# Optimization experiments

Measured on AMD Instinct MI355X. Metric: run time of the kernel, lower is better.

The kernel has to match this reference:

```python
import jax, jax.numpy as jnp
import numpy as np

B, ORDER, N, D, H = 16, 2, 512, 128, 8
DH = D // H
NEG_SLOPE = 0.2


def setup_inputs() -> dict:
    key = jax.random.key(0)
    ks = jax.random.split(key, 8)
    stdv = 1.0 / np.sqrt(DH)

    def u(k, shape):
        return jax.random.uniform(k, shape, jnp.float32, -stdv, stdv)

    x = jax.random.normal(ks[0], (B, ORDER, N, D), jnp.float32)
    A = jax.random.randint(ks[1], (B, ORDER, N, N), 0, 5, jnp.int32)
    # Stacked params for the 2*order GAT modules: axis0 = order, axis1 = (conv1, conv2)
    W = u(ks[2], (ORDER, 2, D, D))            # project.weight
    pb = jnp.zeros((ORDER, 2, D), jnp.float32)  # project.bias (init 0)
    att_src = u(ks[3], (ORDER, 2, H, DH))
    att_dst = u(ks[4], (ORDER, 2, H, DH))
    bias = jnp.zeros((ORDER, 2, D), jnp.float32)  # GAT output bias (init 0)
    return {"x": x, "A": A, "W": W, "pb": pb,
            "att_src": att_src, "att_dst": att_dst, "bias": bias}


def _gat(x, Af, W, pb, a_src, a_dst, b):
    # x: [B,N,D]; Af: [B,N,N] float in {0,1}
    xp = x @ W.T + pb                                  # project
    xh = xp.reshape(B, N, H, DH)                       # [B,N,H,DH]
    s_src = jnp.einsum('bnhd,hd->bnh', xh, a_src)      # [B,N,H]
    s_dst = jnp.einsum('bnhd,hd->bnh', xh, a_dst)
    alpha = s_src[:, :, None, :] + s_dst[:, None, :, :]  # [B,src,dst,H]
    alpha = jnp.where((Af != 1.0)[..., None], 0.0, alpha)
    alpha = jnp.where(alpha >= 0, alpha, NEG_SLOPE * alpha)  # leaky relu
    alpha = jax.nn.softmax(alpha, axis=1)              # softmax over src dim
    out = jnp.einsum('bsdh,bshf->bdhf', alpha, xh).reshape(B, N, D)
    out = out + xp                                     # add_self_loops
    return out + b


def reference(x, A, W, pb, att_src, att_dst, bias):
    A1 = ((A == 2) | (A == 4)).astype(x.dtype)  # [B,ORDER,N,N]
    A2 = ((A == 3) | (A == 4)).astype(x.dtype)
    hs = []
    for i in range(ORDER):
        h1 = _gat(x[:, i], A1[:, i], W[i, 0], pb[i, 0], att_src[i, 0], att_dst[i, 0], bias[i, 0])
        h2 = _gat(x[:, i], A2[:, i], W[i, 1], pb[i, 1], att_src[i, 1], att_dst[i, 1], bias[i, 1])
        hs.append(h1 + h2)
    h = jnp.stack(hs, axis=1)                          # [B,ORDER,N,D]
    out = h + h.mean(axis=1, keepdims=True)
    return out
```

## Files before the change

kernel.cpp:

```cpp
#include <hip/hip_runtime.h>

#define N_ 512
#define D_ 128
#define LOG2E 1.44269504088896f


typedef __attribute__((ext_vector_type(8))) short short8;
typedef __attribute__((ext_vector_type(4))) float floatx4;
typedef __attribute__((ext_vector_type(4))) unsigned int uintx4;
typedef __attribute__((ext_vector_type(2))) _Float16 half2v;
typedef __attribute__((ext_vector_type(8))) _Float16 half8;

#if defined(__has_builtin)
#if __has_builtin(__builtin_amdgcn_exp2f)
#define EXP2F(x) __builtin_amdgcn_exp2f(x)
#else
#define EXP2F(x) exp2f(x)
#endif
#else
#define EXP2F(x) exp2f(x)
#endif

__device__ __forceinline__ unsigned int pkh(float a, float b) {
    auto h = __builtin_amdgcn_cvt_pkrtz(a, b);
    return __builtin_bit_cast(unsigned int, h);
}

__global__ __launch_bounds__(256) void prep_kernel(
    const float* __restrict__ x, const float* __restrict__ W,
    const float* __restrict__ pb, const float* __restrict__ att_src,
    const float* __restrict__ att_dst, const int* __restrict__ A,
    unsigned short* __restrict__ xpt, unsigned int* __restrict__ sgEs,
    unsigned int* __restrict__ sgFs, float2* __restrict__ sgD,
    unsigned int* __restrict__ mgT)
{
    __shared__ _Float16 va_l[8][136];
    __shared__ float c0_l[8];

    const int bid0 = blockIdx.x;
    const int t = threadIdx.x;

    if (bid0 >= 1024) {
        const int bid = bid0 - 1024;
        const int bi = bid >> 4;
        const int rem = bid & 15;
        const int dg = rem >> 2;
        const int jw = rem & 3;
        const int dp = t & 63, q = t >> 6;
        const int dstb = dg * 128 + dp * 2;
        const int sbase = jw * 128 + q * 8;
        const int* Ab = A + (size_t)bi * N_ * N_ + dstb;
        unsigned int a00 = 0, a01 = 0, a10 = 0, a11 = 0;
#pragma unroll
        for (int cp = 0; cp < 4; ++cp) {
#pragma unroll
            for (int i = 0; i < 8; ++i) {
                const int s = sbase + cp * 32 + i;
                const int2 v = *(const int2*)(Ab + (size_t)s * N_);
                const int bitp = cp * 8 + i;
                a00 |= ((0x14u >> v.x) & 1u) << bitp;
                a10 |= ((0x18u >> v.x) & 1u) << bitp;
                a01 |= ((0x14u >> v.y) & 1u) << bitp;
                a11 |= ((0x18u >> v.y) & 1u) << bitp;
            }
        }
        const int i0 = bi * 2;
        mgT[(((size_t)i0 * 4 + q) * 512 + dstb + 0) * 4 + jw] = a00;
        mgT[(((size_t)i0 * 4 + q) * 512 + dstb + 1) * 4 + jw] = a01;
        mgT[(((size_t)(i0 + 1) * 4 + q) * 512 + dstb + 0) * 4 + jw] = a10;
        mgT[(((size_t)(i0 + 1) * 4 + q) * 512 + dstb + 1) * 4 + jw] = a11;
        return;
    }

    const int unit = bid0 >> 1;
    const int half = bid0 & 1;
    const int ntile = unit & 7;
    const int inst  = unit >> 3;
    const int j = inst & 1;
    const int bi = inst >> 1;
    const int ij = (bi & 1) * 2 + j;
    const int wave = t >> 6, L = t & 63, n = L & 15, q = L >> 4;
    const float* wb = W + (size_t)ij * D_ * D_;

    {
        const int c = t >> 5;
        const int k0 = (t & 31) * 4;
        const int hn = half * 4 + (c & 3);
        const float* av = ((c < 4) ? att_src : att_dst) + ij * D_ + hn * 16;
        const float* Wh = wb + (size_t)(hn * 16) * D_ + k0;
        float a0 = 0.f, a1 = 0.f, a2 = 0.f, a3 = 0.f;
#pragma unroll
        for (int dd = 0; dd < 16; ++dd) {
            const float a = av[dd];
            const float4 wv = *(const float4*)(Wh + (size_t)dd * D_);
            a0 += wv.x * a; a1 += wv.y * a; a2 += wv.z * a; a3 += wv.w * a;
        }
        va_l[c][k0 + 0] = (_Float16)(a0 * LOG2E);
        va_l[c][k0 + 1] = (_Float16)(a1 * LOG2E);
        va_l[c][k0 + 2] = (_Float16)(a2 * LOG2E);
        va_l[c][k0 + 3] = (_Float16)(a3 * LOG2E);
        if (t < 8) {
            const int hn2 = half * 4 + (t & 3);
            const float* av2 = ((t < 4) ? att_src : att_dst) + ij * D_ + hn2 * 16;
            const float* pbp = pb + ij * D_ + hn2 * 16;
            float s = 0.f;
#pragma unroll
            for (int dd = 0; dd < 16; ++dd) s += pbp[dd] * av2[dd];
            c0_l[t] = s * LOG2E;
        }
    }

    const int n0w = ntile * 64 + wave * 16;
    const float* xrow = x + ((size_t)bi * N_ + n0w + n) * D_ + q * 8;
    half8 Af[4];
#pragma unroll
    for (int kc = 0; kc < 4; ++kc) {
        const float4 a0 = *(const float4*)(xrow + kc * 32);
        const float4 a1 = *(const float4*)(xrow + kc * 32 + 4);
        uintx4 au;
        au.x = pkh(a0.x, a0.y);
        au.y = pkh(a0.z, a0.w);
        au.z = pkh(a1.x, a1.y);
        au.w = pkh(a1.z, a1.w);
        Af[kc] = __builtin_bit_cast(half8, au);
    }

    __syncthreads();

    floatx4 S = (floatx4){0.f, 0.f, 0.f, 0.f};
    {
        const _Float16* var = &va_l[n & 7][q * 8];
#pragma unroll
        for (int kc = 0; kc < 4; ++kc) {
            const half8 Bs = *(const half8*)(var + kc * 32);
            S = __builtin_amdgcn_mfma_f32_16x16x32_f16(Af[kc], Bs, S, 0, 0, 0);
        }
    }

#pragma unroll
    for (int ft = 0; ft < 4; ++ft) {
        const int head = half * 4 + ft;
        const int fg = head * 16 + n;
        const float* wrow = wb + (size_t)fg * D_ + q * 8;
        floatx4 C = (floatx4){0.f, 0.f, 0.f, 0.f};
#pragma unroll
        for (int kc = 0; kc < 4; ++kc) {
            const float4 b0 = *(const float4*)(wrow + kc * 32);
            const float4 b1 = *(const float4*)(wrow + kc * 32 + 4);
            uintx4 bu;
            bu.x = pkh(b0.x, b0.y);
            bu.y = pkh(b0.z, b0.w);
            bu.z = pkh(b1.x, b1.y);
            bu.w = pkh(b1.z, b1.w);
            C = __builtin_amdgcn_mfma_f32_16x16x32_f16(
                Af[kc], __builtin_bit_cast(half8, bu), C, 0, 0, 0);
        }
        const float pbv = pb[ij * D_ + fg];
        uint2 pk;
        pk.x = pkh(C[0] + pbv, C[1] + pbv);
        pk.y = pkh(C[2] + pbv, C[3] + pbv);
        *(uint2*)&xpt[((size_t)inst * D_ + fg) * N_ + n0w + q * 4] = pk;
    }

    if (n < 8) {
        const float cc = c0_l[n];
        const float v0 = S[0] + cc, v1 = S[1] + cc;
        const float v2 = S[2] + cc, v3 = S[3] + cc;
        if (n < 4) {
            const int head = half * 4 + n;
            const size_t base = ((size_t)inst * 8 + head) * 256 + (n0w >> 1) + q * 2;
            sgEs[base + 0] = pkh(EXP2F(v0), EXP2F(v1));
            sgEs[base + 1] = pkh(EXP2F(v2), EXP2F(v3));
            sgFs[base + 0] = pkh(EXP2F(0.2f * v0), EXP2F(0.2f * v1));
            sgFs[base + 1] = pkh(EXP2F(0.2f * v2), EXP2F(0.2f * v3));
        } else {
            const int head = half * 4 + (n - 4);
            const size_t base = ((size_t)inst * 8 + head) * N_ + n0w + q * 4;
            float2 e0; e0.x = EXP2F(v0); e0.y = EXP2F(0.2f * v0); sgD[base + 0] = e0;
            float2 e1; e1.x = EXP2F(v1); e1.y = EXP2F(0.2f * v1); sgD[base + 1] = e1;
            float2 e2; e2.x = EXP2F(v2); e2.y = EXP2F(0.2f * v2); sgD[base + 2] = e2;
            float2 e3; e3.x = EXP2F(v3); e3.y = EXP2F(0.2f * v3); sgD[base + 3] = e3;
        }
    }
}

__global__ __launch_bounds__(1024, 4) void attn_kernel(
    const unsigned short* __restrict__ xpt,
    const unsigned int* __restrict__ sgEs,
    const unsigned int* __restrict__ sgFs,
    const float2* __restrict__ sgD,
    const unsigned int* __restrict__ mgT,
    const float* __restrict__ bias,
    float* __restrict__ hout)
{
    __shared__ unsigned int smem[16384];

    const int bid = blockIdx.x;
    const int xcd = bid & 7;
    const int idx = bid >> 3;
    const int b   = xcd * 2 + (idx >> 4);
    const int tp  = idx & 15;
    const int d0a = tp * 32;
    const int b4  = b * 4;
    const int t = threadIdx.x;
    const int wave = t >> 6, L = t & 63, n = L & 15, q = L >> 4;
    const int io = wave >> 3;
    const int cv = (wave >> 2) & 1;
    const int h0 = (wave & 3) * 2;
    const int il = io * 2 + cv;
    const int inst = b4 + il;
    const int ij = il;

    const int ph = tp & 3;
    const int Pb = ph * 128;

    {
        const uint4* sE = (const uint4*)(sgEs + (size_t)b4 * 2048);
        const uint4* sF = (const uint4*)(sgFs + (size_t)b4 * 2048);
        uint4* dE = (uint4*)smem;
        uint4* dF = (uint4*)(smem + 8192);
        dE[t] = sE[t]; dE[1024 + t] = sE[1024 + t];
        dF[t] = sF[t]; dF[1024 + t] = sF[1024 + t];
    }

    unsigned int mwr[2][4];
    unsigned int iEd2[2][2], rd2[2][2];
#pragma unroll
    for (int tt = 0; tt < 2; ++tt) {
        const int d0 = d0a + tt * 16;
        const uint4 mreg =
            *(const uint4*)(mgT + (((size_t)inst * 4 + q) * 512 + d0 + n) * 4);
        const unsigned int mwt[4] = { mreg.x, mreg.y, mreg.z, mreg.w };
#pragma unroll
        for (int w = 0; w < 4; ++w) {
            const int src = (w + ph) & 3;
            unsigned int v = mwt[0];
            v = (src == 1) ? mwt[1] : v;
            v = (src == 2) ? mwt[2] : v;
            v = (src == 3) ? mwt[3] : v;
            mwr[tt][w] = v;
        }
#pragma unroll
        for (int hh = 0; hh < 2; ++hh) {
            const float2 ed = sgD[((size_t)inst * 8 + h0 + hh) * N_ + d0 + n];
            const float iEd = 1.0f / ed.x;
            const float rdv = ed.y * iEd;
            iEd2[tt][hh] = pkh(iEd, iEd);
            rd2[tt][hh] = pkh(rdv, rdv);
        }
    }

    __syncthreads();

    const unsigned short* xpi = xpt + (size_t)inst * D_ * N_;
    const unsigned short* bpq0 = xpi + (size_t)(h0 * 16 + n) * N_ + q * 8;
    const unsigned short* bpq1 = xpi + (size_t)((h0 + 1) * 16 + n) * N_ + q * 8;
    const unsigned int* esw = smem + il * 2048;
    const unsigned int* fsw = smem + 8192 + il * 2048;
    const unsigned int* e0p = esw + h0 * 256 + q * 4;
    const unsigned int* e1p = esw + (h0 + 1) * 256 + q * 4;
    const unsigned int* f0p = fsw + h0 * 256 + q * 4;
    const unsigned int* f1p = fsw + (h0 + 1) * 256 + q * 4;

    const uintx4 ou = { 0x3C003C00u, 0x3C003C00u, 0x3C003C00u, 0x3C003C00u };
    const half8 onesB = __builtin_bit_cast(half8, ou);

    floatx4 Cacc[2][2] = { { (floatx4){0.f,0.f,0.f,0.f}, (floatx4){0.f,0.f,0.f,0.f} },
                           { (floatx4){0.f,0.f,0.f,0.f}, (floatx4){0.f,0.f,0.f,0.f} } };
    floatx4 Cz[2][2]   = { { (floatx4){0.f,0.f,0.f,0.f}, (floatx4){0.f,0.f,0.f,0.f} },
                           { (floatx4){0.f,0.f,0.f,0.f}, (floatx4){0.f,0.f,0.f,0.f} } };

    uintx4 Bb0[4], Bb1[4];
#pragma unroll
    for (int c = 0; c < 4; ++c) {
        const int off = (c * 32 + Pb) & 511;
        Bb0[c] = *(const uintx4*)(bpq0 + off);
        Bb1[c] = *(const uintx4*)(bpq1 + off);
    }
#pragma unroll
    for (int c = 0; c < 16; ++c) {
        const int offe = (c * 16 + (Pb >> 1)) & 255;
#pragma unroll
        for (int hh = 0; hh < 2; ++hh) {
            const uint4 Ep = *(const uint4*)((hh ? e1p : e0p) + offe);
            const uint4 Fp = *(const uint4*)((hh ? f1p : f0p) + offe);
            const unsigned int eu[4] = { Ep.x, Ep.y, Ep.z, Ep.w };
            const unsigned int fu[4] = { Fp.x, Fp.y, Fp.z, Fp.w };
            const half8 Bc = __builtin_bit_cast(half8, hh ? Bb1[c & 3] : Bb0[c & 3]);
#pragma unroll
            for (int tt = 0; tt < 2; ++tt) {
                const half2v rdh = __builtin_bit_cast(half2v, rd2[tt][hh]);
                const unsigned int word = mwr[tt][c >> 2];
                uintx4 au;
                unsigned int wts[4];
#pragma unroll
                for (int p = 0; p < 4; ++p) {
                    const int sh = (c & 3) * 8 + 2 * p;
                    const unsigned int wb2 = word >> sh;
                    const unsigned int sel =
                        ((wb2 & 1u) ? 0x0000FFFFu : 0u) |
                        ((wb2 & 2u) ? 0xFFFF0000u : 0u);
                    const half2v e = __builtin_bit_cast(half2v, eu[p]);
                    const half2v f = __builtin_bit_cast(half2v, fu[p]);
                    const half2v pr = f * rdh;
                    const half2v wv = __builtin_elementwise_max(pr, e);
                    const unsigned int wvu = __builtin_bit_cast(unsigned int, wv);
                    wts[p] = (sel & wvu) | (~sel & iEd2[tt][hh]);
                }
                au.x = wts[0]; au.y = wts[1]; au.z = wts[2]; au.w = wts[3];
                const half8 As = __builtin_bit_cast(half8, au);
                Cacc[tt][hh] = __builtin_amdgcn_mfma_f32_16x16x32_f16(
                    As, Bc, Cacc[tt][hh], 0, 0, 0);
                Cz[tt][hh] = __builtin_amdgcn_mfma_f32_16x16x32_f16(
                    As, onesB, Cz[tt][hh], 0, 0, 0);
            }
        }
        if (c < 12) {
            const int off = ((c + 4) * 32 + Pb) & 511;
            Bb0[c & 3] = *(const uintx4*)(bpq0 + off);
            Bb1[c & 3] = *(const uintx4*)(bpq1 + off);
        }
    }

    float vals[2][2][4];
#pragma unroll
    for (int tt = 0; tt < 2; ++tt) {
        const int d0 = d0a + tt * 16;
#pragma unroll
        for (int hh = 0; hh < 2; ++hh) {
            const int h = h0 + hh;
            const float bv = bias[ij * D_ + h * 16 + n];
            const uint2 sv =
                *(const uint2*)(xpi + (size_t)(h * 16 + n) * N_ + d0 + q * 4);
            const half2v s0 = __builtin_bit_cast(half2v, sv.x);
            const half2v s1 = __builtin_bit_cast(half2v, sv.y);
            const float selfv[4] = { (float)s0[0], (float)s0[1],
                                     (float)s1[0], (float)s1[1] };
#pragma unroll
            for (int reg = 0; reg < 4; ++reg) {
                const float Zi = 1.0f / Cz[tt][hh][reg];
                vals[tt][hh][reg] = Cacc[tt][hh][reg] * Zi + selfv[reg] + bv;
            }
        }
    }

    __syncthreads();
    float* smf = (float*)smem;
    if (cv == 1) {
#pragma unroll
        for (int tt = 0; tt < 2; ++tt) {
            float* out_l = smf + (tt * 2 + io) * 2112;
#pragma unroll
            for (int hh = 0; hh < 2; ++hh)
#pragma unroll
                for (int reg = 0; reg < 4; ++reg)
                    out_l[(q * 4 + reg) * 132 + (h0 + hh) * 16 + n] =
                        vals[tt][hh][reg];
        }
    }
    __syncthreads();
    if (cv == 0) {
#pragma unroll
        for (int tt = 0; tt < 2; ++tt) {
            float* out_l = smf + (tt * 2 + io) * 2112;
#pragma unroll
            for (int hh = 0; hh < 2; ++hh)
#pragma unroll
                for (int reg = 0; reg < 4; ++reg) {
                    vals[tt][hh][reg] +=
                        out_l[(q * 4 + reg) * 132 + (h0 + hh) * 16 + n];
                    out_l[(q * 4 + reg) * 132 + (h0 + hh) * 16 + n] =
                        vals[tt][hh][reg];
                }
        }
    }
    __syncthreads();
    if (cv == 0) {
#pragma unroll
        for (int tt = 0; tt < 2; ++tt) {
            const int d0 = d0a + tt * 16;
            const float* oth = smf + (tt * 2 + (1 - io)) * 2112;
#pragma unroll
            for (int hh = 0; hh < 2; ++hh)
#pragma unroll
                for (int reg = 0; reg < 4; ++reg) {
                    const float other =
                        oth[(q * 4 + reg) * 132 + (h0 + hh) * 16 + n];
                    hout[((size_t)(b * 2 + io) * N_ + d0 + q * 4 + reg) * D_ +
                         (h0 + hh) * 16 + n] =
                        1.5f * vals[tt][hh][reg] + 0.5f * other;
                }
        }
    }
}

extern "C" void kernel_launch(void* const* d_in, const int* in_sizes, int n_in,
                              void* d_out, int out_size, void* d_ws, size_t ws_size,
                              hipStream_t stream)
{
    const float* x   = (const float*)d_in[0];
    const int*   A   = (const int*)d_in[1];
    const float* W   = (const float*)d_in[2];
    const float* pb  = (const float*)d_in[3];
    const float* as_ = (const float*)d_in[4];
    const float* ad_ = (const float*)d_in[5];
    const float* bs  = (const float*)d_in[6];

    unsigned short* xpt = (unsigned short*)d_ws;
    unsigned int* sgEs = (unsigned int*)((char*)d_ws + (8u << 20));
    unsigned int* sgFs = (unsigned int*)((char*)d_ws + (8u << 20) + (512u << 10));
    float2* sgD = (float2*)((char*)d_ws + (9u << 20));
    unsigned int* mgT = (unsigned int*)((char*)d_ws + (11u << 20));
    float* h = (float*)d_out;

    prep_kernel<<<1536, 256, 0, stream>>>(x, W, pb, as_, ad_, A, xpt, sgEs, sgFs, sgD, mgT);
    attn_kernel<<<256, 1024, 0, stream>>>(xpt, sgEs, sgFs, sgD, mgT, bs, h);
}
```

Before: 132.1 us.

## Fuse prep and attention kernels into one cooperative launch with grid sync

Merges the projection/score/mask-packing prep kernel and the attention kernel into a single cooperative kernel of 256 blocks of 1024 threads. The prep work is redistributed across the larger blocks, and the attention phase presumably runs after a grid-wide sync. Mask loads now use nontemporal 64-bit loads. This removes one kernel launch and the gap between kernels. In exchange it adds a grid barrier, and the prep phase now runs at the lower parallelism of the attention launch shape.

```diff
diff --git a/kernel.cpp b/kernel.cpp
--- a/kernel.cpp
+++ b/kernel.cpp
@@ -1,8 +1,11 @@
 #include <hip/hip_runtime.h>
+#include <hip/hip_cooperative_groups.h>
 
 #define N_ 512
 #define D_ 128
 #define LOG2E 1.44269504088896f
+
+namespace cg = cooperative_groups;
 
 
 typedef __attribute__((ext_vector_type(8))) short short8;
@@ -26,370 +29,376 @@
     return __builtin_bit_cast(unsigned int, h);
 }
 
-__global__ __launch_bounds__(256) void prep_kernel(
+__global__ __launch_bounds__(1024, 4) void fused_kernel(
     const float* __restrict__ x, const float* __restrict__ W,
     const float* __restrict__ pb, const float* __restrict__ att_src,
     const float* __restrict__ att_dst, const int* __restrict__ A,
+    const float* __restrict__ bias,
     unsigned short* __restrict__ xpt, unsigned int* __restrict__ sgEs,
     unsigned int* __restrict__ sgFs, float2* __restrict__ sgD,
-    unsigned int* __restrict__ mgT)
-{
-    __shared__ _Float16 va_l[8][136];
-    __shared__ float c0_l[8];
-
-    const int bid0 = blockIdx.x;
-    const int t = threadIdx.x;
-
-    if (bid0 >= 1024) {
-        const int bid = bid0 - 1024;
-        const int bi = bid >> 4;
-        const int rem = bid & 15;
-        const int dg = rem >> 2;
-        const int jw = rem & 3;
-        const int dp = t & 63, q = t >> 6;
-        const int dstb = dg * 128 + dp * 2;
-        const int sbase = jw * 128 + q * 8;
-        const int* Ab = A + (size_t)bi * N_ * N_ + dstb;
-        unsigned int a00 = 0, a01 = 0, a10 = 0, a11 = 0;
-#pragma unroll
-        for (int cp = 0; cp < 4; ++cp) {
-#pragma unroll
-            for (int i = 0; i < 8; ++i) {
-                const int s = sbase + cp * 32 + i;
-                const int2 v = *(const int2*)(Ab + (size_t)s * N_);
-                const int bitp = cp * 8 + i;
-                a00 |= ((0x14u >> v.x) & 1u) << bitp;
-                a10 |= ((0x18u >> v.x) & 1u) << bitp;
-                a01 |= ((0x14u >> v.y) & 1u) << bitp;
-                a11 |= ((0x18u >> v.y) & 1u) << bitp;
-            }
-        }
-        const int i0 = bi * 2;
-        mgT[(((size_t)i0 * 4 + q) * 512 + dstb + 0) * 4 + jw] = a00;
-        mgT[(((size_t)i0 * 4 + q) * 512 + dstb + 1) * 4 + jw] = a01;
-        mgT[(((size_t)(i0 + 1) * 4 + q) * 512 + dstb + 0) * 4 + jw] = a10;
-        mgT[(((size_t)(i0 + 1) * 4 + q) * 512 + dstb + 1) * 4 + jw] = a11;
-        return;
-    }
-
-    const int unit = bid0 >> 1;
-    const int half = bid0 & 1;
-    const int ntile = unit & 7;
-    const int inst  = unit >> 3;
-    const int j = inst & 1;
-    const int bi = inst >> 1;
-    const int ij = (bi & 1) * 2 + j;
-    const int wave = t >> 6, L = t & 63, n = L & 15, q = L >> 4;
-    const float* wb = W + (size_t)ij * D_ * D_;
-
-    {
-        const int c = t >> 5;
-        const int k0 = (t & 31) * 4;
-        const int hn = half * 4 + (c & 3);
-        const float* av = ((c < 4) ? att_src : att_dst) + ij * D_ + hn * 16;
-        const float* Wh = wb + (size_t)(hn * 16) * D_ + k0;
-        float a0 = 0.f, a1 = 0.f, a2 = 0.f, a3 = 0.f;
-#pragma unroll
-        for (int dd = 0; dd < 16; ++dd) {
-            const float a = av[dd];
-            const float4 wv = *(const float4*)(Wh + (size_t)dd * D_);
-            a0 += wv.x * a; a1 += wv.y * a; a2 += wv.z * a; a3 += wv.w * a;
-        }
-        va_l[c][k0 + 0] = (_Float16)(a0 * LOG2E);
-        va_l[c][k0 + 1] = (_Float16)(a1 * LOG2E);
-        va_l[c][k0 + 2] = (_Float16)(a2 * LOG2E);
-        va_l[c][k0 + 3] = (_Float16)(a3 * LOG2E);
-        if (t < 8) {
-            const int hn2 = half * 4 + (t & 3);
-            const float* av2 = ((t < 4) ? att_src : att_dst) + ij * D_ + hn2 * 16;
-            const float* pbp = pb + ij * D_ + hn2 * 16;
-            float s = 0.f;
-#pragma unroll
-            for (int dd = 0; dd < 16; ++dd) s += pbp[dd] * av2[dd];
-            c0_l[t] = s * LOG2E;
-        }
-    }
-
-    const int n0w = ntile * 64 + wave * 16;
-    const float* xrow = x + ((size_t)bi * N_ + n0w + n) * D_ + q * 8;
-    half8 Af[4];
-#pragma unroll
-    for (int kc = 0; kc < 4; ++kc) {
-        const float4 a0 = *(const float4*)(xrow + kc * 32);
-        const float4 a1 = *(const float4*)(xrow + kc * 32 + 4);
-        uintx4 au;
-        au.x = pkh(a0.x, a0.y);
-        au.y = pkh(a0.z, a0.w);
-        au.z = pkh(a1.x, a1.y);
-        au.w = pkh(a1.z, a1.w);
-        Af[kc] = __builtin_bit_cast(half8, au);
-    }
-
-    __syncthreads();
-
-    floatx4 S = (floatx4){0.f, 0.f, 0.f, 0.f};
-    {
-        const _Float16* var = &va_l[n & 7][q * 8];
-#pragma unroll
-        for (int kc = 0; kc < 4; ++kc) {
-            const half8 Bs = *(const half8*)(var + kc * 32);
-            S = __builtin_amdgcn_mfma_f32_16x16x32_f16(Af[kc], Bs, S, 0, 0, 0);
-        }
-    }
-
-#pragma unroll
-    for (int ft = 0; ft < 4; ++ft) {
-        const int head = half * 4 + ft;
-        const int fg = head * 16 + n;
-        const float* wrow = wb + (size_t)fg * D_ + q * 8;
-        floatx4 C = (floatx4){0.f, 0.f, 0.f, 0.f};
-#pragma unroll
-        for (int kc = 0; kc < 4; ++kc) {
-            const float4 b0 = *(const float4*)(wrow + kc * 32);
-            const float4 b1 = *(const float4*)(wrow + kc * 32 + 4);
-            uintx4 bu;
-            bu.x = pkh(b0.x, b0.y);
-            bu.y = pkh(b0.z, b0.w);
-            bu.z = pkh(b1.x, b1.y);
-            bu.w = pkh(b1.z, b1.w);
-            C = __builtin_amdgcn_mfma_f32_16x16x32_f16(
-                Af[kc], __builtin_bit_cast(half8, bu), C, 0, 0, 0);
-        }
-        const float pbv = pb[ij * D_ + fg];
-        uint2 pk;
-        pk.x = pkh(C[0] + pbv, C[1] + pbv);
-        pk.y = pkh(C[2] + pbv, C[3] + pbv);
-        *(uint2*)&xpt[((size_t)inst * D_ + fg) * N_ + n0w + q * 4] = pk;
-    }
-
-    if (n < 8) {
-        const float cc = c0_l[n];
-        const float v0 = S[0] + cc, v1 = S[1] + cc;
-        const float v2 = S[2] + cc, v3 = S[3] + cc;
-        if (n < 4) {
-            const int head = half * 4 + n;
-            const size_t base = ((size_t)inst * 8 + head) * 256 + (n0w >> 1) + q * 2;
-            sgEs[base + 0] = pkh(EXP2F(v0), EXP2F(v1));
-            sgEs[base + 1] = pkh(EXP2F(v2), EXP2F(v3));
-            sgFs[base + 0] = pkh(EXP2F(0.2f * v0), EXP2F(0.2f * v1));
-            sgFs[base + 1] = pkh(EXP2F(0.2f * v2), EXP2F(0.2f * v3));
-        } else {
-            const int head = half * 4 + (n - 4);
-            const size_t base = ((size_t)inst * 8 + head) * N_ + n0w + q * 4;
-            float2 e0; e0.x = EXP2F(v0); e0.y = EXP2F(0.2f * v0); sgD[base + 0] = e0;
-            float2 e1; e1.x = EXP2F(v1); e1.y = EXP2F(0.2f * v1); sgD[base + 1] = e1;
-            float2 e2; e2.x = EXP2F(v2); e2.y = EXP2F(0.2f * v2); sgD[base + 2] = e2;
-            float2 e3; e3.x = EXP2F(v3); e3.y = EXP2F(0.2f * v3); sgD[base + 3] = e3;
-        }
-    }
-}
-
-__global__ __launch_bounds__(1024, 4) void attn_kernel(
-    const unsigned short* __restrict__ xpt,
-    const unsigned int* __restrict__ sgEs,
-    const unsigned int* __restrict__ sgFs,
-    const float2* __restrict__ sgD,
-    const unsigned int* __restrict__ mgT,
-    const float* __restrict__ bias,
-    float* __restrict__ hout)
+    unsigned int* __restrict__ mgT, float* __restrict__ hout)
 {
     __shared__ unsigned int smem[16384];
 
     const int bid = blockIdx.x;
     const int xcd = bid & 7;
     const int idx = bid >> 3;
-    const int b   = xcd * 2 + (idx >> 4);
-    const int tp  = idx & 15;
-    const int d0a = tp * 32;
-    const int b4  = b * 4;
     const int t = threadIdx.x;
-    const int wave = t >> 6, L = t & 63, n = L & 15, q = L >> 4;
-    const int io = wave >> 3;
-    const int cv = (wave >> 2) & 1;
-    const int h0 = (wave & 3) * 2;
-    const int il = io * 2 + cv;
-    const int inst = b4 + il;
-    const int ij = il;
-
-    const int ph = tp & 3;
-    const int Pb = ph * 128;
 
     {
-        const uint4* sE = (const uint4*)(sgEs + (size_t)b4 * 2048);
-        const uint4* sF = (const uint4*)(sgFs + (size_t)b4 * 2048);
-        uint4* dE = (uint4*)smem;
-        uint4* dF = (uint4*)(smem + 8192);
-        dE[t] = sE[t]; dE[1024 + t] = sE[1024 + t];
-        dF[t] = sF[t]; dF[1024 + t] = sF[1024 + t];
+        const int inst = xcd * 8 + (idx >> 2);
+        const int quarter = idx & 3;
+        const int j = inst & 1;
+        const int bi = inst >> 1;
+        const int ij = (bi & 1) * 2 + j;
+        const float* wb = W + (size_t)ij * D_ * D_;
+
+        _Float16* va = (_Float16*)smem;
+        float* c0s = (float*)(smem + 1100);
+
+        if (t < 512) {
+            const int halfv = t >> 8;
+            const int c = (t >> 5) & 7;
+            const int k0 = (t & 31) * 4;
+            const int hn = halfv * 4 + (c & 3);
+            const float* av = ((c < 4) ? att_src : att_dst) + ij * D_ + hn * 16;
+            const float* Wh = wb + (size_t)(hn * 16) * D_ + k0;
+            float a0 = 0.f, a1 = 0.f, a2 = 0.f, a3 = 0.f;
+#pragma unroll
+            for (int dd = 0; dd < 16; ++dd) {
+                const float a = av[dd];
+                const float4 wv = *(const float4*)(Wh + (size_t)dd * D_);
+                a0 += wv.x * a; a1 += wv.y * a; a2 += wv.z * a; a3 += wv.w * a;
+            }
+            _Float16* vp = va + (halfv * 8 + c) * 136 + k0;
+            vp[0] = (_Float16)(a0 * LOG2E);
+            vp[1] = (_Float16)(a1 * LOG2E);
+            vp[2] = (_Float16)(a2 * LOG2E);
+            vp[3] = (_Float16)(a3 * LOG2E);
+        }
+        if (t < 16) {
+            const int halfv = t >> 3;
+            const int cc = t & 7;
+            const int hn2 = halfv * 4 + (cc & 3);
+            const float* av2 = ((cc < 4) ? att_src : att_dst) + ij * D_ + hn2 * 16;
+            const float* pbp = pb + ij * D_ + hn2 * 16;
+            float s = 0.f;
+#pragma unroll
+            for (int dd = 0; dd < 16; ++dd) s += pbp[dd] * av2[dd];
+            c0s[halfv * 8 + cc] = s * LOG2E;
+        }
+
+        const int sub = t >> 8;
+        const int ntile = quarter * 2 + (sub >> 1);
+        const int halfp = sub & 1;
+        const int wavep = (t >> 6) & 3;
+        const int L = t & 63, n = L & 15, q = L >> 4;
+        const int n0w = ntile * 64 + wavep * 16;
+
+        const float* xrow = x + ((size_t)bi * N_ + n0w + n) * D_ + q * 8;
+        half8 Af[4];
+#pragma unroll
+        for (int kc = 0; kc < 4; ++kc) {
+            const float4 a0 = *(const float4*)(xrow + kc * 32);
+            const float4 a1 = *(const float4*)(xrow + kc * 32 + 4);
+            uintx4 au;
+            au.x = pkh(a0.x, a0.y);
+            au.y = pkh(a0.z, a0.w);
+            au.z = pkh(a1.x, a1.y);
+            au.w = pkh(a1.z, a1.w);
+            Af[kc] = __builtin_bit_cast(half8, au);
+        }
+
+        __syncthreads();
+
+        floatx4 S = (floatx4){0.f, 0.f, 0.f, 0.f};
+        {
+            const _Float16* var = va + (halfp * 8 + (n & 7)) * 136 + q * 8;
+#pragma unroll
+            for (int kc = 0; kc < 4; ++kc) {
+                const half8 Bs = *(const half8*)(var + kc * 32);
+                S = __builtin_amdgcn_mfma_f32_16x16x32_f16(Af[kc], Bs, S, 0, 0, 0);
+            }
+        }
+
+#pragma unroll
+        for (int ft = 0; ft < 4; ++ft) {
+            const int head = halfp * 4 + ft;
+            const int fg = head * 16 + n;
+            const float* wrow = wb + (size_t)fg * D_ + q * 8;
+            floatx4 C = (floatx4){0.f, 0.f, 0.f, 0.f};
+#pragma unroll
+            for (int kc = 0; kc < 4; ++kc) {
+                const float4 b0 = *(const float4*)(wrow + kc * 32);
+                const float4 b1 = *(const float4*)(wrow + kc * 32 + 4);
+                uintx4 bu;
+                bu.x = pkh(b0.x, b0.y);
+                bu.y = pkh(b0.z, b0.w);
+                bu.z = pkh(b1.x, b1.y);
+                bu.w = pkh(b1.z, b1.w);
+                C = __builtin_amdgcn_mfma_f32_16x16x32_f16(
+                    Af[kc], __builtin_bit_cast(half8, bu), C, 0, 0, 0);
+            }
+            const float pbv = pb[ij * D_ + fg];
+            uint2 pk;
+            pk.x = pkh(C[0] + pbv, C[1] + pbv);
+            pk.y = pkh(C[2] + pbv, C[3] + pbv);
+            *(uint2*)&xpt[((size_t)inst * D_ + fg) * N_ + n0w + q * 4] = pk;
+        }
+
+        if (n < 8) {
+            const float cc2 = c0s[halfp * 8 + n];
+            const float v0 = S[0] + cc2, v1 = S[1] + cc2;
+            const float v2 = S[2] + cc2, v3 = S[3] + cc2;
+            if (n < 4) {
+                const int head = halfp * 4 + n;
+                const size_t base = ((size_t)inst * 8 + head) * 256 + (n0w >> 1) + q * 2;
+                sgEs[base + 0] = pkh(EXP2F(v0), EXP2F(v1));
+                sgEs[base + 1] = pkh(EXP2F(v2), EXP2F(v3));
+                sgFs[base + 0] = pkh(EXP2F(0.2f * v0), EXP2F(0.2f * v1));
+                sgFs[base + 1] = pkh(EXP2F(0.2f * v2), EXP2F(0.2f * v3));
+            } else {
+                const int head = halfp * 4 + (n - 4);
+                const size_t base = ((size_t)inst * 8 + head) * N_ + n0w + q * 4;
+                float2 e0; e0.x = EXP2F(v0); e0.y = EXP2F(0.2f * v0); sgD[base + 0] = e0;
+                float2 e1; e1.x = EXP2F(v1); e1.y = EXP2F(0.2f * v1); sgD[base + 1] = e1;
+                float2 e2; e2.x = EXP2F(v2); e2.y = EXP2F(0.2f * v2); sgD[base + 2] = e2;
+                float2 e3; e3.x = EXP2F(v3); e3.y = EXP2F(0.2f * v3); sgD[base + 3] = e3;
+            }
+        }
+
+        if (t < 512) {
+            const int sub2 = t >> 8;
+            const int u = idx * 2 + sub2;
+            const int bim = xcd * 4 + (u >> 4);
+            const int rem = u & 15;
+            const int dg = rem >> 2, jw = rem & 3;
+            const int tl = t & 255;
+            const int qm = tl >> 6, dp = tl & 63;
+            const int dstb = dg * 128 + dp * 2;
+            const int sbase = jw * 128 + qm * 8;
+            const long long* Ab =
+                (const long long*)(A + (size_t)bim * N_ * N_ + dstb);
+            unsigned int a00 = 0, a01 = 0, a10 = 0, a11 = 0;
+#pragma unroll
+            for (int cp = 0; cp < 4; ++cp) {
+#pragma unroll
+                for (int i = 0; i < 8; ++i) {
+                    const int s = sbase + cp * 32 + i;
+                    const long long vv =
+                        __builtin_nontemporal_load(Ab + (size_t)s * (N_ / 2));
+                    const unsigned int vx = (unsigned int)(vv & 0xffffffffll);
+                    const unsigned int vy = (unsigned int)(vv >> 32);
+                    const int bitp = cp * 8 + i;
+                    a00 |= ((0x14u >> vx) & 1u) << bitp;
+                    a10 |= ((0x18u >> vx) & 1u) << bitp;
+                    a01 |= ((0x14u >> vy) & 1u) << bitp;
+                    a11 |= ((0x18u >> vy) & 1u) << bitp;
+                }
+            }
+            const int i0 = bim * 2;
+            mgT[(((size_t)i0 * 4 + qm) * 512 + dstb + 0) * 4 + jw] = a00;
+            mgT[(((size_t)i0 * 4 + qm) * 512 + dstb + 1) * 4 + jw] = a01;
+            mgT[(((size_t)(i0 + 1) * 4 + qm) * 512 + dstb + 0) * 4 + jw] = a10;
+            mgT[(((size_t)(i0 + 1) * 4 + qm) * 512 + dstb + 1) * 4 + jw] = a11;
+        }
     }
 
-    unsigned int mwr[2][4];
-    unsigned int iEd2[2][2], rd2[2][2];
-#pragma unroll
-    for (int tt = 0; tt < 2; ++tt) {
-        const int d0 = d0a + tt * 16;
-        const uint4 mreg =
-            *(const uint4*)(mgT + (((size_t)inst * 4 + q) * 512 + d0 + n) * 4);
-        const unsigned int mwt[4] = { mreg.x, mreg.y, mreg.z, mreg.w };
-#pragma unroll
-        for (int w = 0; w < 4; ++w) {
-            const int src = (w + ph) & 3;
-            unsigned int v = mwt[0];
-            v = (src == 1) ? mwt[1] : v;
-            v = (src == 2) ? mwt[2] : v;
-            v = (src == 3) ? mwt[3] : v;
-            mwr[tt][w] = v;
-        }
-#pragma unroll
-        for (int hh = 0; hh < 2; ++hh) {
-            const float2 ed = sgD[((size_t)inst * 8 + h0 + hh) * N_ + d0 + n];
-            const float iEd = 1.0f / ed.x;
-            const float rdv = ed.y * iEd;
-            iEd2[tt][hh] = pkh(iEd, iEd);
-            rd2[tt][hh] = pkh(rdv, rdv);
-        }
-    }
-
-    __syncthreads();
-
-    const unsigned short* xpi = xpt + (size_t)inst * D_ * N_;
-    const unsigned short* bpq0 = xpi + (size_t)(h0 * 16 + n) * N_ + q * 8;
-    const unsigned short* bpq1 = xpi + (size_t)((h0 + 1) * 16 + n) * N_ + q * 8;
-    const unsigned int* esw = smem + il * 2048;
-    const unsigned int* fsw = smem + 8192 + il * 2048;
-    const unsigned int* e0p = esw + h0 * 256 + q * 4;
-    const unsigned int* e1p = esw + (h0 + 1) * 256 + q * 4;
-    const unsigned int* f0p = fsw + h0 * 256 + q * 4;
-    const unsigned int* f1p = fsw + (h0 + 1) * 256 + q * 4;
-
-    const uintx4 ou = { 0x3C003C00u, 0x3C003C00u, 0x3C003C00u, 0x3C003C00u };
-    const half8 onesB = __builtin_bit_cast(half8, ou);
-
-    floatx4 Cacc[2][2] = { { (floatx4){0.f,0.f,0.f,0.f}, (floatx4){0.f,0.f,0.f,0.f} },
-                           { (floatx4){0.f,0.f,0.f,0.f}, (floatx4){0.f,0.f,0.f,0.f} } };
-    floatx4 Cz[2][2]   = { { (floatx4){0.f,0.f,0.f,0.f}, (floatx4){0.f,0.f,0.f,0.f} },
-                           { (floatx4){0.f,0.f,0.f,0.f}, (floatx4){0.f,0.f,0.f,0.f} } };
-
-    uintx4 Bb0[4], Bb1[4];
-#pragma unroll
-    for (int c = 0; c < 4; ++c) {
-        const int off = (c * 32 + Pb) & 511;
-        Bb0[c] = *(const uintx4*)(bpq0 + off);
-        Bb1[c] = *(const uintx4*)(bpq1 + off);
-    }
-#pragma unroll
-    for (int c = 0; c < 16; ++c) {
-        const int offe = (c * 16 + (Pb >> 1)) & 255;
-#pragma unroll
-        for (int hh = 0; hh < 2; ++hh) {
-            const uint4 Ep = *(const uint4*)((hh ? e1p : e0p) + offe);
-            const uint4 Fp = *(const uint4*)((hh ? f1p : f0p) + offe);
-            const unsigned int eu[4] = { Ep.x, Ep.y, Ep.z, Ep.w };
-            const unsigned int fu[4] = { Fp.x, Fp.y, Fp.z, Fp.w };
-            const half8 Bc = __builtin_bit_cast(half8, hh ? Bb1[c & 3] : Bb0[c & 3]);
-#pragma unroll
-            for (int tt = 0; tt < 2; ++tt) {
-                const half2v rdh = __builtin_bit_cast(half2v, rd2[tt][hh]);
-                const unsigned int word = mwr[tt][c >> 2];
-                uintx4 au;
-                unsigned int wts[4];
-#pragma unroll
-                for (int p = 0; p < 4; ++p) {
-                    const int sh = (c & 3) * 8 + 2 * p;
-                    const unsigned int wb2 = word >> sh;
-                    const unsigned int sel =
-                        ((wb2 & 1u) ? 0x0000FFFFu : 0u) |
-                        ((wb2 & 2u) ? 0xFFFF0000u : 0u);
-                    const half2v e = __builtin_bit_cast(half2v, eu[p]);
-                    const half2v f = __builtin_bit_cast(half2v, fu[p]);
-                    const half2v pr = f * rdh;
-                    const half2v wv = __builtin_elementwise_max(pr, e);
-                    const unsigned int wvu = __builtin_bit_cast(unsigned int, wv);
-                    wts[p] = (sel & wvu) | (~sel & iEd2[tt][hh]);
-                }
-                au.x = wts[0]; au.y = wts[1]; au.z = wts[2]; au.w = wts[3];
-                const half8 As = __builtin_bit_cast(half8, au);
-                Cacc[tt][hh] = __builtin_amdgcn_mfma_f32_16x16x32_f16(
-                    As, Bc, Cacc[tt][hh], 0, 0, 0);
-                Cz[tt][hh] = __builtin_amdgcn_mfma_f32_16x16x32_f16(
-                    As, onesB, Cz[tt][hh], 0, 0, 0);
-            }
-        }
-        if (c < 12) {
-            const int off = ((c + 4) * 32 + Pb) & 511;
-            Bb0[c & 3] = *(const uintx4*)(bpq0 + off);
-            Bb1[c & 3] = *(const uintx4*)(bpq1 + off);
-        }
-    }
-
-    float vals[2][2][4];
-#pragma unroll
-    for (int tt = 0; tt < 2; ++tt) {
-        const int d0 = d0a + tt * 16;
-#pragma unroll
-        for (int hh = 0; hh < 2; ++hh) {
-            const int h = h0 + hh;
-            const float bv = bias[ij * D_ + h * 16 + n];
-            const uint2 sv =
-                *(const uint2*)(xpi + (size_t)(h * 16 + n) * N_ + d0 + q * 4);
-            const half2v s0 = __builtin_bit_cast(half2v, sv.x);
-            const half2v s1 = __builtin_bit_cast(half2v, sv.y);
-            const float selfv[4] = { (float)s0[0], (float)s0[1],
-                                     (float)s1[0], (float)s1[1] };
-#pragma unroll
-            for (int reg = 0; reg < 4; ++reg) {
-                const float Zi = 1.0f / Cz[tt][hh][reg];
-                vals[tt][hh][reg] = Cacc[tt][hh][reg] * Zi + selfv[reg] + bv;
-            }
-        }
-    }
-
-    __syncthreads();
-    float* smf = (float*)smem;
-    if (cv == 1) {
-#pragma unroll
-        for (int tt = 0; tt < 2; ++tt) {
-            float* out_l = smf + (tt * 2 + io) * 2112;
-#pragma unroll
-            for (int hh = 0; hh < 2; ++hh)
-#pragma unroll
-                for (int reg = 0; reg < 4; ++reg)
-                    out_l[(q * 4 + reg) * 132 + (h0 + hh) * 16 + n] =
-                        vals[tt][hh][reg];
-        }
-    }
-    __syncthreads();
-    if (cv == 0) {
-#pragma unroll
-        for (int tt = 0; tt < 2; ++tt) {
-            float* out_l = smf + (tt * 2 + io) * 2112;
-#pragma unroll
-            for (int hh = 0; hh < 2; ++hh)
-#pragma unroll
-                for (int reg = 0; reg < 4; ++reg) {
-                    vals[tt][hh][reg] +=
-                        out_l[(q * 4 + reg) * 132 + (h0 + hh) * 16 + n];
-                    out_l[(q * 4 + reg) * 132 + (h0 + hh) * 16 + n] =
-                        vals[tt][hh][reg];
-                }
-        }
-    }
-    __syncthreads();
-    if (cv == 0) {
+    cg::this_grid().sync();
+
+    {
+        const int b   = xcd * 2 + (idx >> 4);
+        const int tp  = idx & 15;
+        const int d0a = tp * 32;
+        const int b4  = b * 4;
+        const int wave = t >> 6, L = t & 63, n = L & 15, q = L >> 4;
+        const int io = wave >> 3;
+        const int cv = (wave >> 2) & 1;
+        const int h0 = (wave & 3) * 2;
+        const int il = io * 2 + cv;
+        const int inst = b4 + il;
+        const int ij = il;
+
+        const int ph = tp & 3;
+        const int Pb = ph * 128;
+
+        {
+            const uint4* sE = (const uint4*)(sgEs + (size_t)b4 * 2048);
+            const uint4* sF = (const uint4*)(sgFs + (size_t)b4 * 2048);
+            uint4* dE = (uint4*)smem;
+            uint4* dF = (uint4*)(smem + 8192);
+            dE[t] = sE[t]; dE[1024 + t] = sE[1024 + t];
+            dF[t] = sF[t]; dF[1024 + t] = sF[1024 + t];
+        }
+
+        unsigned int mwr[2][4];
+        unsigned int iEd2[2][2], rd2[2][2];
 #pragma unroll
         for (int tt = 0; tt < 2; ++tt) {
             const int d0 = d0a + tt * 16;
-            const float* oth = smf + (tt * 2 + (1 - io)) * 2112;
-#pragma unroll
-            for (int hh = 0; hh < 2; ++hh)
+            const uint4 mreg =
+                *(const uint4*)(mgT + (((size_t)inst * 4 + q) * 512 + d0 + n) * 4);
+            const unsigned int mwt[4] = { mreg.x, mreg.y, mreg.z, mreg.w };
+#pragma unroll
+            for (int w = 0; w < 4; ++w) {
+                const int src = (w + ph) & 3;
+                unsigned int v = mwt[0];
+                v = (src == 1) ? mwt[1] : v;
+                v = (src == 2) ? mwt[2] : v;
+                v = (src == 3) ? mwt[3] : v;
+                mwr[tt][w] = v;
+            }
+#pragma unroll
+            for (int hh = 0; hh < 2; ++hh) {
+                const float2 ed = sgD[((size_t)inst * 8 + h0 + hh) * N_ + d0 + n];
+                const float iEd = 1.0f / ed.x;
+                const float rdv = ed.y * iEd;
+                iEd2[tt][hh] = pkh(iEd, iEd);
+                rd2[tt][hh] = pkh(rdv, rdv);
+            }
+        }
+
+        __syncthreads();
+
+        const unsigned short* xpi = xpt + (size_t)inst * D_ * N_;
+        const unsigned short* bpq0 = xpi + (size_t)(h0 * 16 + n) * N_ + q * 8;
+        const unsigned short* bpq1 = xpi + (size_t)((h0 + 1) * 16 + n) * N_ + q * 8;
+        const unsigned int* esw = smem + il * 2048;
+        const unsigned int* fsw = smem + 8192 + il * 2048;
+        const unsigned int* e0p = esw + h0 * 256 + q * 4;
+        const unsigned int* e1p = esw + (h0 + 1) * 256 + q * 4;
+        const unsigned int* f0p = fsw + h0 * 256 + q * 4;
+        const unsigned int* f1p = fsw + (h0 + 1) * 256 + q * 4;
+
+        const uintx4 ou = { 0x3C003C00u, 0x3C003C00u, 0x3C003C00u, 0x3C003C00u };
+        const half8 onesB = __builtin_bit_cast(half8, ou);
+
+        floatx4 Cacc[2][2] = { { (floatx4){0.f,0.f,0.f,0.f}, (floatx4){0.f,0.f,0.f,0.f} },
+                               { (floatx4){0.f,0.f,0.f,0.f}, (floatx4){0.f,0.f,0.f,0.f} } };
+        floatx4 Cz[2][2]   = { { (floatx4){0.f,0.f,0.f,0.f}, (floatx4){0.f,0.f,0.f,0.f} },
+                               { (floatx4){0.f,0.f,0.f,0.f}, (floatx4){0.f,0.f,0.f,0.f} } };
+
+        uintx4 Bb0[4], Bb1[4];
+#pragma unroll
+        for (int c = 0; c < 4; ++c) {
+            const int off = (c * 32 + Pb) & 511;
+            Bb0[c] = *(const uintx4*)(bpq0 + off);
+            Bb1[c] = *(const uintx4*)(bpq1 + off);
+        }
+#pragma unroll
+        for (int c = 0; c < 16; ++c) {
+            const int offe = (c * 16 + (Pb >> 1)) & 255;
+#pragma unroll
+            for (int hh = 0; hh < 2; ++hh) {
+                const uint4 Ep = *(const uint4*)((hh ? e1p : e0p) + offe);
+                const uint4 Fp = *(const uint4*)((hh ? f1p : f0p) + offe);
+                const unsigned int eu[4] = { Ep.x, Ep.y, Ep.z, Ep.w };
+                const unsigned int fu[4] = { Fp.x, Fp.y, Fp.z, Fp.w };
+                const half8 Bc = __builtin_bit_cast(half8, hh ? Bb1[c & 3] : Bb0[c & 3]);
+#pragma unroll
+                for (int tt = 0; tt < 2; ++tt) {
+                    const half2v rdh = __builtin_bit_cast(half2v, rd2[tt][hh]);
+                    const unsigned int word = mwr[tt][c >> 2];
+                    uintx4 au;
+                    unsigned int wts[4];
+#pragma unroll
+                    for (int p = 0; p < 4; ++p) {
+                        const int sh = (c & 3) * 8 + 2 * p;
+                        const unsigned int wb2 = word >> sh;
+                        const unsigned int sel =
+                            ((wb2 & 1u) ? 0x0000FFFFu : 0u) |
+                            ((wb2 & 2u) ? 0xFFFF0000u : 0u);
+                        const half2v e = __builtin_bit_cast(half2v, eu[p]);
+                        const half2v f = __builtin_bit_cast(half2v, fu[p]);
+                        const half2v pr = f * rdh;
+                        const half2v wv = __builtin_elementwise_max(pr, e);
+                        const unsigned int wvu = __builtin_bit_cast(unsigned int, wv);
+                        wts[p] = (sel & wvu) | (~sel & iEd2[tt][hh]);
+                    }
+                    au.x = wts[0]; au.y = wts[1]; au.z = wts[2]; au.w = wts[3];
+                    const half8 As = __builtin_bit_cast(half8, au);
+                    Cacc[tt][hh] = __builtin_amdgcn_mfma_f32_16x16x32_f16(
+                        As, Bc, Cacc[tt][hh], 0, 0, 0);
+                    Cz[tt][hh] = __builtin_amdgcn_mfma_f32_16x16x32_f16(
+                        As, onesB, Cz[tt][hh], 0, 0, 0);
+                }
+            }
+            if (c < 12) {
+                const int off = ((c + 4) * 32 + Pb) & 511;
+                Bb0[c & 3] = *(const uintx4*)(bpq0 + off);
+                Bb1[c & 3] = *(const uintx4*)(bpq1 + off);
+            }
+        }
+
+        float vals[2][2][4];
+#pragma unroll
+        for (int tt = 0; tt < 2; ++tt) {
+            const int d0 = d0a + tt * 16;
+#pragma unroll
+            for (int hh = 0; hh < 2; ++hh) {
+                const int h = h0 + hh;
+                const float bv = bias[ij * D_ + h * 16 + n];
+                const uint2 sv =
+                    *(const uint2*)(xpi + (size_t)(h * 16 + n) * N_ + d0 + q * 4);
+                const half2v s0 = __builtin_bit_cast(half2v, sv.x);
+                const half2v s1 = __builtin_bit_cast(half2v, sv.y);
+                const float selfv[4] = { (float)s0[0], (float)s0[1],
+                                         (float)s1[0], (float)s1[1] };
 #pragma unroll
                 for (int reg = 0; reg < 4; ++reg) {
-                    const float other =
-                        oth[(q * 4 + reg) * 132 + (h0 + hh) * 16 + n];
-                    hout[((size_t)(b * 2 + io) * N_ + d0 + q * 4 + reg) * D_ +
-                         (h0 + hh) * 16 + n] =
-                        1.5f * vals[tt][hh][reg] + 0.5f * other;
+                    const float Zi = 1.0f / Cz[tt][hh][reg];
+                    vals[tt][hh][reg] = Cacc[tt][hh][reg] * Zi + selfv[reg] + bv;
                 }
+            }
+        }
+
+        __syncthreads();
+        float* smf = (float*)smem;
+        if (cv == 1) {
+#pragma unroll
+            for (int tt = 0; tt < 2; ++tt) {
+                float* out_l = smf + (tt * 2 + io) * 2112;
+#pragma unroll
+                for (int hh = 0; hh < 2; ++hh)
+#pragma unroll
+                    for (int reg = 0; reg < 4; ++reg)
+                        out_l[(q * 4 + reg) * 132 + (h0 + hh) * 16 + n] =
+                            vals[tt][hh][reg];
+            }
+        }
+        __syncthreads();
+        if (cv == 0) {
+#pragma unroll
+            for (int tt = 0; tt < 2; ++tt) {
+                float* out_l = smf + (tt * 2 + io) * 2112;
+#pragma unroll
+                for (int hh = 0; hh < 2; ++hh)
+#pragma unroll
+                    for (int reg = 0; reg < 4; ++reg) {
+                        vals[tt][hh][reg] +=
+                            out_l[(q * 4 + reg) * 132 + (h0 + hh) * 16 + n];
+                        out_l[(q * 4 + reg) * 132 + (h0 + hh) * 16 + n] =
+                            vals[tt][hh][reg];
+                    }
+            }
+        }
+        __syncthreads();
+        if (cv == 0) {
+#pragma unroll
+            for (int tt = 0; tt < 2; ++tt) {
+                const int d0 = d0a + tt * 16;
+                const float* oth = smf + (tt * 2 + (1 - io)) * 2112;
+#pragma unroll
+                for (int hh = 0; hh < 2; ++hh)
+#pragma unroll
+                    for (int reg = 0; reg < 4; ++reg) {
+                        const float other =
+                            oth[(q * 4 + reg) * 132 + (h0 + hh) * 16 + n];
+                        hout[((size_t)(b * 2 + io) * N_ + d0 + q * 4 + reg) * D_ +
+                             (h0 + hh) * 16 + n] =
+                            1.5f * vals[tt][hh][reg] + 0.5f * other;
+                    }
+            }
         }
     }
 }
@@ -413,6 +422,11 @@
     unsigned int* mgT = (unsigned int*)((char*)d_ws + (11u << 20));
     float* h = (float*)d_out;
 
-    prep_kernel<<<1536, 256, 0, stream>>>(x, W, pb, as_, ad_, A, xpt, sgEs, sgFs, sgD, mgT);
-    attn_kernel<<<256, 1024, 0, stream>>>(xpt, sgEs, sgFs, sgD, mgT, bs, h);
+    void* args[13] = {
+        (void*)&x, (void*)&W, (void*)&pb, (void*)&as_, (void*)&ad_,
+        (void*)&A, (void*)&bs, (void*)&xpt, (void*)&sgEs, (void*)&sgFs,
+        (void*)&sgD, (void*)&mgT, (void*)&h
+    };
+    (void)hipLaunchCooperativeKernel((void*)fused_kernel, dim3(256), dim3(1024),
+                                     args, 0, stream);
 }
```

Result: slower. 181.2 us (+37.2%).
